# Kernel tuning notes

Hardware: AMD Instinct MI355X
Metric: run time of the kernel (lower is better)

The kernel has to match this reference:

```python
import jax, jax.numpy as jnp
import numpy as np

B, Hd, Wd, C, NH, WS = 8, 128, 128, 192, 6, 8
HDIM = int(C * 2.0)   # FFN hidden = 384
RED = C // 8          # AIM channel-gate reduction = 24


def setup_inputs() -> dict:
    key = jax.random.key(0)
    ks = jax.random.split(key, 12)
    s = 0.02
    return {
        "x": jax.random.normal(ks[0], (B, Hd * Wd, C), jnp.float32),
        "H": Hd,
        "W": Wd,
        "n1_w": jnp.ones((C,), jnp.float32),
        "n1_b": jnp.zeros((C,), jnp.float32),
        "qkv_w": jax.random.normal(ks[1], (C, 3 * C), jnp.float32) * s,
        "proj_w": jax.random.normal(ks[2], (C, C), jnp.float32) * s,
        "proj_b": jnp.zeros((C,), jnp.float32),
        "attn_bias": jax.random.normal(ks[3], (NH, WS * WS, WS * WS), jnp.float32) * s,
        "conv_w": jax.random.normal(ks[4], (C, 1, 3, 3), jnp.float32) * s,
        "cg_w1": jax.random.normal(ks[5], (RED, C), jnp.float32) * s,
        "cg_w2": jax.random.normal(ks[6], (C, RED), jnp.float32) * s,
        "n2_w": jnp.ones((C,), jnp.float32),
        "n2_b": jnp.zeros((C,), jnp.float32),
        "fc1_w": jax.random.normal(ks[7], (C, HDIM), jnp.float32) * s,
        "smix_w": jax.random.normal(ks[8], (HDIM, 1, 3, 3), jnp.float32) * s,
        "fc2_w": jax.random.normal(ks[9], (HDIM, C), jnp.float32) * s,
    }


def _ln(x, w, b):
    m = x.mean(-1, keepdims=True)
    v = ((x - m) ** 2).mean(-1, keepdims=True)
    return (x - m) * jax.lax.rsqrt(v + 1e-5) * w + b


def _dwconv(x, w, H, W):
    # x: [B, L, Cx] -> depthwise 3x3 'same' conv -> [B, L, Cx]
    Bx, L, Cx = x.shape
    xi = x.transpose(0, 2, 1).reshape(Bx, Cx, H, W)
    y = jax.lax.conv_general_dilated(
        xi, w, (1, 1), 'SAME', feature_group_count=Cx,
        dimension_numbers=('NCHW', 'OIHW', 'NCHW'))
    return y.reshape(Bx, Cx, L).transpose(0, 2, 1)


def _window_attn(x, H, W, qkv_w, proj_w, proj_b, bias):
    Bx, L, Cx = x.shape
    nHw, nWw = H // WS, W // WS  # H, W are multiples of WS here (no padding needed)
    hd = Cx // NH
    # [B, L, C] -> [B*nH*nW, ws*ws, C]
    xw = (x.reshape(Bx, nHw, WS, nWw, WS, Cx)
           .transpose(0, 1, 3, 2, 4, 5)
           .reshape(Bx * nHw * nWw, WS * WS, Cx))
    qkv = (xw @ qkv_w).reshape(-1, WS * WS, 3, NH, hd).transpose(2, 0, 3, 1, 4)
    q, k, v = qkv[0], qkv[1], qkv[2]          # [Bw, nh, N, hd]
    logits = (q * hd ** -0.5) @ k.transpose(0, 1, 3, 2) + bias[None]
    attn = jax.nn.softmax(logits, axis=-1)
    out = (attn @ v).transpose(0, 2, 1, 3).reshape(-1, WS * WS, Cx)
    out = out @ proj_w + proj_b
    # windows -> [B, L, C]
    return (out.reshape(Bx, nHw, nWw, WS, WS, Cx)
               .transpose(0, 1, 3, 2, 4, 5)
               .reshape(Bx, L, Cx))


def reference(x, H, W, n1_w, n1_b, qkv_w, proj_w, proj_b, attn_bias,
              conv_w, cg_w1, cg_w2, n2_w, n2_b, fc1_w, smix_w, fc2_w):
    n1 = _ln(x, n1_w, n1_b)
    attn_feat = _window_attn(n1, H, W, qkv_w, proj_w, proj_b, attn_bias)
    conv_feat = jax.nn.gelu(_dwconv(n1, conv_w, H, W), approximate=False)
    # AIM: channel_modulates_spatial (btype == 'spatial')
    pooled = conv_feat.mean(axis=1)                                   # [B, C]
    cm = jax.nn.sigmoid(jax.nn.gelu(pooled @ cg_w1.T, approximate=False) @ cg_w2.T)
    x = x + attn_feat * cm[:, None, :] + conv_feat                    # residual (DropPath=id)
    # FFN with depthwise spatial mixing
    n2 = _ln(x, n2_w, n2_b)
    h = jax.nn.gelu(n2 @ fc1_w, approximate=False)                    # [B, L, HDIM]
    h = _dwconv(h, smix_w, H, W)
    return x + h @ fc2_w
```

## Files before the change

### kernel.cpp

```cpp
#include <hip/hip_runtime.h>
#include <hip/hip_bf16.h>
#include <math.h>

#define BATCH 8
#define CCH 192
#define LTOK 16384
#define BL 131072LL
#define NWIN 2048
#define NHEADS 6

typedef __hip_bfloat16 bf16;
typedef __bf16 bfr;
typedef bfr bf16x8 __attribute__((ext_vector_type(8)));
typedef float f32x4 __attribute__((ext_vector_type(4)));
typedef unsigned short u16x8 __attribute__((ext_vector_type(8)));
typedef unsigned short u16x4 __attribute__((ext_vector_type(4)));
typedef unsigned int u32x2 __attribute__((ext_vector_type(2)));

#define FX     0
#define FN1W   1
#define FN1B   2
#define FQKVW  3
#define FPROJW 4
#define FPROJB 5
#define FBIAS  6
#define FCONVW 7
#define FCG1   8
#define FCG2   9
#define FN2W   10
#define FN2B   11
#define FFC1   12
#define FSMIX  13
#define FFC2   14

struct InPtrs { const void* p[15]; int n[15]; };

__device__ __forceinline__ float ldin(const void* p, long long i, int f32) {
    return f32 ? ((const float*)p)[i]
               : __bfloat162float(((const bf16*)p)[i]);
}

__device__ __forceinline__ float bfcvt(unsigned short u) {
    return __uint_as_float((unsigned)u << 16);
}

__device__ __forceinline__ f32x4 ld4f(const void* p, long long i, int f32) {
    if (f32) return *(const f32x4*)((const float*)p + i);
    u16x4 v = *(const u16x4*)((const bf16*)p + i);
    f32x4 r;
    r[0] = bfcvt(v[0]); r[1] = bfcvt(v[1]); r[2] = bfcvt(v[2]); r[3] = bfcvt(v[3]);
    return r;
}
__device__ __forceinline__ f32x4 ld4b(const bf16* p, long long i) {
    u16x4 v = *(const u16x4*)(p + i);
    f32x4 r;
    r[0] = bfcvt(v[0]); r[1] = bfcvt(v[1]); r[2] = bfcvt(v[2]); r[3] = bfcvt(v[3]);
    return r;
}
__device__ __forceinline__ void st4b(bf16* p, long long i, f32x4 v) {
    union { bf16 h; unsigned short u; } cv;
    u16x4 o;
    cv.h = __float2bfloat16(v[0]); o[0] = cv.u;
    cv.h = __float2bfloat16(v[1]); o[1] = cv.u;
    cv.h = __float2bfloat16(v[2]); o[2] = cv.u;
    cv.h = __float2bfloat16(v[3]); o[3] = cv.u;
    *(u16x4*)(p + i) = o;
}

__device__ __forceinline__ unsigned pk2bf(float a, float b) {
    union { bf16 h; unsigned short u; } ca, cb;
    ca.h = __float2bfloat16(a);
    cb.h = __float2bfloat16(b);
    return (unsigned)ca.u | ((unsigned)cb.u << 16);
}

__device__ __forceinline__ float gelu_f(float v) {
    return 0.5f * v * (1.0f + erff(v * 0.70710678118654752f));
}

__global__ void probe_k(InPtrs in, int* flags) {
    __shared__ int s_insane, s_evennz, s_oddnz;
    if (threadIdx.x == 0) { s_insane = 0; s_evennz = 0; s_oddnz = 0; }
    __syncthreads();
    int t = blockIdx.x;
    const bf16* p = (const bf16*)in.p[t];
    int n = in.n[t];
    int m = n < 2048 ? n : 2048;
    bool insane = false, evennz = false, oddnz = false;
    for (int i = threadIdx.x; i < m; i += 256) {
        float v = __bfloat162float(p[i]);
        if (!(fabsf(v) <= 1e9f)) insane = true;
        if (v != 0.0f) { if (i & 1) oddnz = true; else evennz = true; }
    }
    if (insane) s_insane = 1;
    if (evennz) s_evennz = 1;
    if (oddnz)  s_oddnz = 1;
    __syncthreads();
    if (threadIdx.x == 0)
        flags[t] = (s_insane || (!s_evennz && s_oddnz)) ? 1 : 0;
}

__global__ void transpose_k(const void* __restrict__ W, bf16* __restrict__ WT,
                            int K, int N, const int* flag) {
    int f = *flag;
    int idx = blockIdx.x * 256 + threadIdx.x;
    if (idx >= K * N) return;
    int k = idx / N, n = idx % N;
    WT[(long long)n * K + k] = __float2bfloat16(ldin(W, idx, f));
}

__global__ void convw_k(const void* __restrict__ W, float* __restrict__ WT,
                        int CX, const int* flag) {
    int f = *flag;
    int idx = blockIdx.x * 256 + threadIdx.x;
    if (idx >= CX * 9) return;
    int c = idx / 9, t = idx - c * 9;
    WT[t * CX + c] = ldin(W, idx, f);
}

__global__ __launch_bounds__(256)
void ln_kernel(const void* __restrict__ x, const void* __restrict__ w,
               const void* __restrict__ b, bf16* __restrict__ out,
               const int* flags) {
    int fx = flags[FX], fw = flags[FN1W], fb = flags[FN1B];
    int wv = threadIdx.x >> 6, lane = threadIdx.x & 63;
    int gw = lane >> 4, l16 = lane & 15;
    long long t = (long long)blockIdx.x * 16 + wv * 4 + gw;
    long long base = t * CCH;
    f32x4 v[3];
#pragma unroll
    for (int k = 0; k < 3; ++k)
        v[k] = ld4f(x, base + l16 * 4 + 64 * k, fx);
    float s = 0.f;
#pragma unroll
    for (int k = 0; k < 3; ++k) s += v[k][0] + v[k][1] + v[k][2] + v[k][3];
    s += __shfl_xor(s, 1); s += __shfl_xor(s, 2);
    s += __shfl_xor(s, 4); s += __shfl_xor(s, 8);
    float mean = s * (1.0f / 192.0f);
    float vs = 0.f;
#pragma unroll
    for (int k = 0; k < 3; ++k)
#pragma unroll
        for (int j = 0; j < 4; ++j) {
            float d = v[k][j] - mean;
            vs += d * d;
        }
    vs += __shfl_xor(vs, 1); vs += __shfl_xor(vs, 2);
    vs += __shfl_xor(vs, 4); vs += __shfl_xor(vs, 8);
    float rstd = rsqrtf(vs * (1.0f / 192.0f) + 1e-5f);
#pragma unroll
    for (int k = 0; k < 3; ++k) {
        int c0 = l16 * 4 + 64 * k;
        f32x4 wv4 = ld4f(w, c0, fw);
        f32x4 bv4 = ld4f(b, c0, fb);
        f32x4 o;
#pragma unroll
        for (int j = 0; j < 4; ++j)
            o[j] = (v[k][j] - mean) * rstd * wv4[j] + bv4[j];
        st4b(out, base + c0, o);
    }
}

template<int EPI, int KK, int NN, typename CT>
__global__ __launch_bounds__(256)
void gemm2_k(const bf16* __restrict__ A_, const bf16* __restrict__ BT_,
             CT* __restrict__ Cmat, const void* __restrict__ bias,
             const float* __restrict__ res, const int* __restrict__ flags) {
    constexpr int KT = KK / 192;
    constexpr int NC = NN / 64;
    constexpr int NITER = NC * KT;
    constexpr int GSTR = KK * 2;
    __shared__ __align__(16) char Ts[64 * 384];

    const int fb = (EPI == 1) ? flags[FPROJB] : 0;
    const int tid = threadIdx.x;
    const int lane = tid & 63, wv = tid >> 6;
    const int r16 = lane & 15, q = lane >> 4;
    const long long m0 = (long long)blockIdx.x * 64;
    const int swz = (r16 & 7) << 4;

    f32x4 pre[6];
    auto loadB = [&](int itn) {
        int nc2 = itn / KT, kt2 = itn - nc2 * KT;
#pragma unroll
        for (int p = 0; p < 6; ++p) {
            int off = p * 4096 + tid * 16;
            int row = off / 384, col = off - row * 384;
            pre[p] = *(const f32x4*)((const char*)BT_ +
                     (long long)(nc2 * 64 + row) * GSTR + kt2 * 384 + col);
        }
    };
    auto writeT = [&]() {
#pragma unroll
        for (int p = 0; p < 6; ++p) {
            int off = p * 4096 + tid * 16;
            int row = off / 384, col = off - row * 384;
            *(f32x4*)(Ts + row * 384 + (col ^ ((row & 7) << 4))) = pre[p];
        }
    };

    loadB(0);

    bf16x8 afrag[KK / 32];
    const char* Arow = Ts + (wv * 16 + r16) * 384;
    const char* asrc = (const char*)(A_ + m0 * KK);
#pragma unroll
    for (int kt = 0; kt < KT; ++kt) {
#pragma unroll
        for (int p = 0; p < 6; ++p) {
            int off = p * 4096 + tid * 16;
            int row = off / 384, col = off - row * 384;
            *(f32x4*)(Ts + row * 384 + (col ^ ((row & 7) << 4))) =
                *(const f32x4*)(asrc + (long long)row * GSTR + kt * 384 + col);
        }
        __syncthreads();
#pragma unroll
        for (int ks = 0; ks < 6; ++ks)
            afrag[kt * 6 + ks] = *(const bf16x8*)(Arow + ((ks * 64 + q * 16) ^ swz));
        __syncthreads();
    }
    writeT();
    __syncthreads();

    f32x4 acc0, acc1, acc2, acc3;
    float resv[16];

    for (int it = 0; it < NITER; ++it) {
        const int nc = it / KT, kt = it - nc * KT;
        if (kt == 0) {
            acc0 = f32x4{0.f, 0.f, 0.f, 0.f};
            acc1 = acc0; acc2 = acc0; acc3 = acc0;
            if (EPI == 3) {
#pragma unroll
                for (int j = 0; j < 4; ++j)
#pragma unroll
                    for (int r = 0; r < 4; ++r)
                        resv[j * 4 + r] =
                            res[(m0 + wv * 16 + q * 4 + r) * NN + nc * 64 + j * 16 + r16];
            }
        }
        const bool nxt = (it + 1 < NITER);
        if (nxt) loadB(it + 1);
#pragma unroll
        for (int ks = 0; ks < 6; ++ks) {
            bf16x8 a = afrag[kt * 6 + ks];
            const char* bb = Ts + r16 * 384 + ((ks * 64 + q * 16) ^ swz);
            bf16x8 b0 = *(const bf16x8*)(bb);
            bf16x8 b1 = *(const bf16x8*)(bb + 16 * 384);
            bf16x8 b2 = *(const bf16x8*)(bb + 32 * 384);
            bf16x8 b3 = *(const bf16x8*)(bb + 48 * 384);
            acc0 = __builtin_amdgcn_mfma_f32_16x16x32_bf16(a, b0, acc0, 0, 0, 0);
            acc1 = __builtin_amdgcn_mfma_f32_16x16x32_bf16(a, b1, acc1, 0, 0, 0);
            acc2 = __builtin_amdgcn_mfma_f32_16x16x32_bf16(a, b2, acc2, 0, 0, 0);
            acc3 = __builtin_amdgcn_mfma_f32_16x16x32_bf16(a, b3, acc3, 0, 0, 0);
        }
        __syncthreads();
        if (nxt) writeT();
        if (kt == KT - 1) {
            f32x4 accs[4] = {acc0, acc1, acc2, acc3};
#pragma unroll
            for (int j = 0; j < 4; ++j) {
                int col = nc * 64 + j * 16 + r16;
#pragma unroll
                for (int r = 0; r < 4; ++r) {
                    long long row = m0 + wv * 16 + q * 4 + r;
                    float v = accs[j][r];
                    if (EPI == 1) v += ldin(bias, col, fb);
                    if (EPI == 2) v = gelu_f(v);
                    if (EPI == 3) v += resv[j * 4 + r];
                    Cmat[row * NN + col] = (CT)v;
                }
            }
        }
        if (nxt) __syncthreads();
    }
}

__global__ __launch_bounds__(384)
void attn_proj_k(const bf16* __restrict__ qkv, const void* __restrict__ bias,
                 const bf16* __restrict__ pwT, const void* __restrict__ proj_b,
                 bf16* __restrict__ attnf, const int* __restrict__ flags) {
    __shared__ __align__(16) bfr Vt[6][32][64];
    __shared__ __align__(16) char PbRaw[6 * 64 * 144];

    const int fbias = flags[FBIAS];
    const int h = threadIdx.x >> 6, lane = threadIdx.x & 63;
    const int w = blockIdx.x;
    const int b = w >> 8, rem = w & 255, wy = rem >> 4, wx = rem & 15;
    const int l15 = lane & 15, quad = lane >> 4;
    const long long tokbase = (long long)b * LTOK + (wy * 8) * 128 + wx * 8;

    bfr (*Pb)[72] = (bfr(*)[72])(PbRaw + h * 64 * 144);

    long long vt = tokbase + (lane >> 3) * 128 + (lane & 7);
    const bfr* vp = (const bfr*)(qkv + vt * 576 + 384 + h * 32);
    bf16x8 v0 = *(const bf16x8*)(vp);
    bf16x8 v1 = *(const bf16x8*)(vp + 8);
    bf16x8 v2 = *(const bf16x8*)(vp + 16);
    bf16x8 v3 = *(const bf16x8*)(vp + 24);

    bf16x8 aq[4], bk[4];
#pragma unroll
    for (int mt = 0; mt < 4; ++mt) {
        int i0 = mt * 16 + l15;
        long long t = tokbase + (i0 >> 3) * 128 + (i0 & 7);
        const bfr* qp = (const bfr*)(qkv + t * 576 + h * 32 + quad * 8);
        aq[mt] = *(const bf16x8*)qp;
        bk[mt] = *(const bf16x8*)(qp + 192);
    }

#pragma unroll
    for (int j = 0; j < 8; ++j) {
        int sc = lane ^ (j << 3);
        Vt[h][j][sc]      = v0[j];
        Vt[h][j + 8][sc]  = v1[j];
        Vt[h][j + 16][sc] = v2[j];
        Vt[h][j + 24][sc] = v3[j];
    }

    f32x4 T[4][4];
#pragma unroll
    for (int ti = 0; ti < 4; ++ti)
#pragma unroll
        for (int tj = 0; tj < 4; ++tj) {
            f32x4 z = {0.f, 0.f, 0.f, 0.f};
            T[ti][tj] = __builtin_amdgcn_mfma_f32_16x16x32_bf16(bk[ti], aq[tj], z, 0, 0, 0);
        }

    const float scale = 0.17677669529663689f;
    const long long bias0 = (long long)h * 4096;
#pragma unroll
    for (int tj = 0; tj < 4; ++tj) {
        const long long brow = bias0 + (tj * 16 + l15) * 64 + quad * 4;
        float mloc = -3.0e38f;
#pragma unroll
        for (int ti = 0; ti < 4; ++ti) {
            f32x4 bv4 = ld4f(bias, brow + ti * 16, fbias);
#pragma unroll
            for (int r = 0; r < 4; ++r) {
                float v = T[ti][tj][r] * scale + bv4[r];
                T[ti][tj][r] = v;
                mloc = fmaxf(mloc, v);
            }
        }
        mloc = fmaxf(mloc, __shfl_xor(mloc, 16));
        mloc = fmaxf(mloc, __shfl_xor(mloc, 32));
        float l = 0.f;
#pragma unroll
        for (int ti = 0; ti < 4; ++ti)
#pragma unroll
            for (int r = 0; r < 4; ++r) {
                float e = __expf(T[ti][tj][r] - mloc);
                T[ti][tj][r] = e;
                l += e;
            }
        l += __shfl_xor(l, 16);
        l += __shfl_xor(l, 32);
        float linv = 1.0f / l;
#pragma unroll
        for (int ti = 0; ti < 4; ++ti) {
            unsigned wlo = pk2bf(T[ti][tj][0] * linv, T[ti][tj][1] * linv);
            unsigned whi = pk2bf(T[ti][tj][2] * linv, T[ti][tj][3] * linv);
            *(u32x2*)&Pb[tj * 16 + l15][ti * 16 + quad * 4] = u32x2{wlo, whi};
        }
    }

    __syncthreads();

    f32x4 O[4][2];
#pragma unroll
    for (int tj = 0; tj < 4; ++tj)
#pragma unroll
        for (int n2 = 0; n2 < 2; ++n2)
            O[tj][n2] = f32x4{0.f, 0.f, 0.f, 0.f};
    const int vsw = (l15 & 7) << 3;
#pragma unroll
    for (int kc = 0; kc < 2; ++kc) {
        bf16x8 bv0 = *(const bf16x8*)&Vt[h][l15][(kc * 32 + quad * 8) ^ vsw];
        bf16x8 bv1 = *(const bf16x8*)&Vt[h][16 + l15][(kc * 32 + quad * 8) ^ vsw];
#pragma unroll
        for (int tj = 0; tj < 4; ++tj) {
            bf16x8 ap = *(const bf16x8*)&Pb[tj * 16 + l15][kc * 32 + quad * 8];
            O[tj][0] = __builtin_amdgcn_mfma_f32_16x16x32_bf16(ap, bv0, O[tj][0], 0, 0, 0);
            O[tj][1] = __builtin_amdgcn_mfma_f32_16x16x32_bf16(ap, bv1, O[tj][1], 0, 0, 0);
        }
    }

    __syncthreads();

    bf16* cat = (bf16*)PbRaw;
#pragma unroll
    for (int tj = 0; tj < 4; ++tj)
#pragma unroll
        for (int n2 = 0; n2 < 2; ++n2)
#pragma unroll
            for (int r = 0; r < 4; ++r)
                cat[(tj * 16 + quad * 4 + r) * 200 + h * 32 + n2 * 16 + l15] =
                    __float2bfloat16(O[tj][n2][r]);

    __syncthreads();

    const int fpb = flags[FPROJB];
    f32x4 pacc[4][2];
#pragma unroll
    for (int mt = 0; mt < 4; ++mt) {
        pacc[mt][0] = f32x4{0.f, 0.f, 0.f, 0.f};
        pacc[mt][1] = pacc[mt][0];
    }
#pragma unroll
    for (int ks = 0; ks < 6; ++ks) {
        bf16x8 af[4];
#pragma unroll
        for (int mt = 0; mt < 4; ++mt)
            af[mt] = *(const bf16x8*)&cat[(mt * 16 + l15) * 200 + ks * 32 + quad * 8];
#pragma unroll
        for (int nt = 0; nt < 2; ++nt) {
            int col = h * 32 + nt * 16 + l15;
            bf16x8 bfr8 = *(const bf16x8*)((const bfr*)pwT + (long long)col * 192 + ks * 32 + quad * 8);
#pragma unroll
            for (int mt = 0; mt < 4; ++mt)
                pacc[mt][nt] = __builtin_amdgcn_mfma_f32_16x16x32_bf16(af[mt], bfr8, pacc[mt][nt], 0, 0, 0);
        }
    }

#pragma unroll
    for (int nt = 0; nt < 2; ++nt) {
        int col = h * 32 + nt * 16 + l15;
        float bv = ldin(proj_b, col, fpb);
#pragma unroll
        for (int mt = 0; mt < 4; ++mt)
#pragma unroll
            for (int r = 0; r < 4; ++r) {
                long long row = (long long)w * 64 + mt * 16 + quad * 4 + r;
                attnf[row * CCH + col] = __float2bfloat16(pacc[mt][nt][r] + bv);
            }
    }
}

template<bool GELU, int CX>
__global__ __launch_bounds__(256)
void dwconv_s4_k(const bf16* __restrict__ in, const float* __restrict__ wt,
                 bf16* __restrict__ out) {
    constexpr int CG = CX / 8;
    int cpx = gridDim.x >> 3;
    int lb = (blockIdx.x & 7) * cpx + (blockIdx.x >> 3);
    long long idx = (long long)lb * 256 + threadIdx.x;
    if (idx >= (BL / 4) * CG) return;
    int cg = (int)(idx % CG);
    long long s = idx / CG;
    int xs = (int)(s & 31);
    long long by = s >> 5;
    int y = (int)(by & 127);
    int x0 = xs * 4;
    int c0 = cg * 8;
    const long long rowpix = by * 128;

    float acc[4][8] = {};
#pragma unroll
    for (int dy = -1; dy <= 1; ++dy) {
        int yy = y + dy;
        if (yy < 0 || yy > 127) continue;
        const bf16* rp = in + ((rowpix + dy * 128) + x0) * CX + c0;
        float fcol[6][8];
#pragma unroll
        for (int ci = 0; ci < 6; ++ci) {
            int xx = x0 + ci - 1;
            if (xx < 0 || xx > 127) {
#pragma unroll
                for (int j = 0; j < 8; ++j) fcol[ci][j] = 0.f;
            } else {
                u16x8 v = *(const u16x8*)(rp + (ci - 1) * CX);
#pragma unroll
                for (int j = 0; j < 8; ++j) fcol[ci][j] = bfcvt(v[j]);
            }
        }
        const float* wb = wt + (dy + 1) * 3 * CX + c0;
#pragma unroll
        for (int dx = 0; dx < 3; ++dx) {
            f32x4 w0 = *(const f32x4*)(wb + dx * CX);
            f32x4 w1 = *(const f32x4*)(wb + dx * CX + 4);
#pragma unroll
            for (int px = 0; px < 4; ++px) {
#pragma unroll
                for (int j = 0; j < 4; ++j) {
                    acc[px][j]     += fcol[px + dx][j]     * w0[j];
                    acc[px][j + 4] += fcol[px + dx][j + 4] * w1[j];
                }
            }
        }
    }
#pragma unroll
    for (int px = 0; px < 4; ++px) {
        __attribute__((aligned(16))) unsigned short ob[8];
#pragma unroll
        for (int j = 0; j < 8; ++j) {
            float vv = acc[px][j];
            if (GELU) vv = gelu_f(vv);
            union { bf16 h; unsigned short u; } cv;
            cv.h = __float2bfloat16(vv);
            ob[j] = cv.u;
        }
        *(u16x8*)(out + (rowpix + x0 + px) * CX + c0) = *(const u16x8*)ob;
    }
}

__global__ __launch_bounds__(192)
void pool_k(const bf16* __restrict__ conv, float* __restrict__ pooled) {
    __shared__ float red[8][192];
    int b = blockIdx.x, chunk = blockIdx.y;
    int cg = threadIdx.x % 24, rr = threadIdx.x / 24;
    float acc[8] = {0.f, 0.f, 0.f, 0.f, 0.f, 0.f, 0.f, 0.f};
    long long rowbase = (long long)b * LTOK + chunk * 256;
    for (int r = rr; r < 256; r += 8) {
        u16x8 v = *(const u16x8*)(conv + (rowbase + r) * CCH + cg * 8);
#pragma unroll
        for (int j = 0; j < 8; ++j) acc[j] += bfcvt(v[j]);
    }
#pragma unroll
    for (int j = 0; j < 8; ++j) red[rr][cg * 8 + j] = acc[j];
    __syncthreads();
    if (rr == 0) {
#pragma unroll
        for (int j = 0; j < 8; ++j) {
            float s = 0.f;
#pragma unroll
            for (int i = 0; i < 8; ++i) s += red[i][cg * 8 + j];
            atomicAdd(&pooled[b * CCH + cg * 8 + j], s);
        }
    }
}

__global__ void cm_k(const float* __restrict__ pooled, const void* __restrict__ w1,
                     const void* __restrict__ w2, float* __restrict__ cm,
                     const int* flags) {
    __shared__ float ps[192], g[24];
    int f1 = flags[FCG1], f2 = flags[FCG2];
    int b = blockIdx.x, c = threadIdx.x;
    ps[c] = pooled[b * CCH + c] * (1.0f / 16384.0f);
    __syncthreads();
    if (c < 24) {
        float t = 0.f;
        for (int k = 0; k < 192; ++k) t += ps[k] * ldin(w1, c * 192 + k, f1);
        g[c] = gelu_f(t);
    }
    __syncthreads();
    float s = 0.f;
#pragma unroll
    for (int r = 0; r < 24; ++r) s += g[r] * ldin(w2, c * 24 + r, f2);
    cm[b * CCH + c] = 1.0f / (1.0f + expf(-s));
}

__global__ __launch_bounds__(256)
void x2ln2_k(const void* __restrict__ x, const bf16* __restrict__ attnf,
             const bf16* __restrict__ conv, const float* __restrict__ cm,
             const void* __restrict__ w, const void* __restrict__ bb,
             float* __restrict__ x2, bf16* __restrict__ n2, const int* flags) {
    int fx = flags[FX], fw = flags[FN2W], fb = flags[FN2B];
    int wv = threadIdx.x >> 6, lane = threadIdx.x & 63;
    int gw = lane >> 4, l16 = lane & 15;
    long long t = (long long)blockIdx.x * 16 + wv * 4 + gw;
    int b = (int)(t >> 14);
    int l = (int)(t & 16383);
    int y = l >> 7, xx = l & 127;
    long long wrow = ((long long)b * 256 + (y >> 3) * 16 + (xx >> 3)) * 64 + (y & 7) * 8 + (xx & 7);

    f32x4 sv[3];
#pragma unroll
    for (int k = 0; k < 3; ++k) {
        int c0 = l16 * 4 + 64 * k;
        f32x4 xv  = ld4f(x, t * CCH + c0, fx);
        f32x4 af  = ld4b(attnf, wrow * CCH + c0);
        f32x4 cf  = ld4b(conv, t * CCH + c0);
        f32x4 cmv = *(const f32x4*)(cm + b * CCH + c0);
        f32x4 o;
#pragma unroll
        for (int j = 0; j < 4; ++j)
            o[j] = xv[j] + af[j] * cmv[j] + cf[j];
        *(f32x4*)(x2 + t * CCH + c0) = o;
        sv[k] = o;
    }
    float s = 0.f;
#pragma unroll
    for (int k = 0; k < 3; ++k) s += sv[k][0] + sv[k][1] + sv[k][2] + sv[k][3];
    s += __shfl_xor(s, 1); s += __shfl_xor(s, 2);
    s += __shfl_xor(s, 4); s += __shfl_xor(s, 8);
    float mean = s * (1.0f / 192.0f);
    float vs = 0.f;
#pragma unroll
    for (int k = 0; k < 3; ++k)
#pragma unroll
        for (int j = 0; j < 4; ++j) {
            float d = sv[k][j] - mean;
            vs += d * d;
        }
    vs += __shfl_xor(vs, 1); vs += __shfl_xor(vs, 2);
    vs += __shfl_xor(vs, 4); vs += __shfl_xor(vs, 8);
    float rstd = rsqrtf(vs * (1.0f / 192.0f) + 1e-5f);
#pragma unroll
    for (int k = 0; k < 3; ++k) {
        int c0 = l16 * 4 + 64 * k;
        f32x4 wv4 = ld4f(w, c0, fw);
        f32x4 bv4 = ld4f(bb, c0, fb);
        f32x4 o;
#pragma unroll
        for (int j = 0; j < 4; ++j)
            o[j] = (sv[k][j] - mean) * rstd * wv4[j] + bv4[j];
        st4b(n2, t * CCH + c0, o);
    }
}

extern "C" void kernel_launch(void* const* d_in, const int* in_sizes, int n_in,
                              void* d_out, int out_size, void* d_ws, size_t ws_size,
                              hipStream_t stream) {
    (void)n_in; (void)out_size; (void)ws_size;
    float* out = (float*)d_out;

    char* wsp = (char*)d_ws;
    size_t off = 0;
    auto alloc = [&](size_t bytes) -> char* {
        char* p = wsp + off;
        off += (bytes + 255) & ~(size_t)255;
        return p;
    };
    int*  flags   = (int*)alloc(15 * 4);
    bf16* qkv_wT  = (bf16*)alloc(576 * 192 * 2);
    bf16* proj_wT = (bf16*)alloc(192 * 192 * 2);
    bf16* fc1_wT  = (bf16*)alloc(384 * 192 * 2);
    bf16* fc2_wT  = (bf16*)alloc(192 * 384 * 2);
    float* convwT = (float*)alloc(9 * CCH * 4);
    float* smixwT = (float*)alloc(9 * 384 * 4);
    float* pooled = (float*)alloc(BATCH * CCH * 4);
    float* cm     = (float*)alloc(BATCH * CCH * 4);
    char* Rbig    = alloc(BL * 576 * 2);
    char* Rpair   = alloc(BL * 384 * 2);

    bf16* qkvb  = (bf16*)Rbig;
    bf16* convf = (bf16*)Rbig;
    bf16* hbuf  = (bf16*)Rbig;
    bf16* n1    = (bf16*)Rpair;
    bf16* attnf = (bf16*)(Rpair + (size_t)BL * 192 * 2);
    bf16* n2    = n1;
    bf16* h2    = (bf16*)Rpair;
    float* x2   = out;

    const int imap[15] = {0, 3, 4, 5, 6, 7, 8, 9, 10, 11, 12, 13, 14, 15, 16};
    InPtrs ip;
    for (int i = 0; i < 15; ++i) { ip.p[i] = d_in[imap[i]]; ip.n[i] = in_sizes[imap[i]]; }
    const void* x        = d_in[0];
    const void* qkv_w    = d_in[5];
    const void* proj_w   = d_in[6];
    const void* proj_b   = d_in[7];
    const void* attnbias = d_in[8];
    const void* conv_w   = d_in[9];
    const void* cg_w1    = d_in[10];
    const void* cg_w2    = d_in[11];
    const void* fc1_w    = d_in[14];
    const void* smix_w   = d_in[15];
    const void* fc2_w    = d_in[16];

    probe_k<<<15, 256, 0, stream>>>(ip, flags);

    transpose_k<<<(192 * 576 + 255) / 256, 256, 0, stream>>>(qkv_w, qkv_wT, 192, 576, flags + FQKVW);
    transpose_k<<<(192 * 192 + 255) / 256, 256, 0, stream>>>(proj_w, proj_wT, 192, 192, flags + FPROJW);
    transpose_k<<<(192 * 384 + 255) / 256, 256, 0, stream>>>(fc1_w, fc1_wT, 192, 384, flags + FFC1);
    transpose_k<<<(384 * 192 + 255) / 256, 256, 0, stream>>>(fc2_w, fc2_wT, 384, 192, flags + FFC2);
    convw_k<<<(CCH * 9 + 255) / 256, 256, 0, stream>>>(conv_w, convwT, CCH, flags + FCONVW);
    convw_k<<<(384 * 9 + 255) / 256, 256, 0, stream>>>(smix_w, smixwT, 384, flags + FSMIX);
    hipMemsetAsync(pooled, 0, BATCH * CCH * 4, stream);

    ln_kernel<<<BL / 16, 256, 0, stream>>>(x, d_in[3], d_in[4], n1, flags);
    gemm2_k<0, 192, 576, bf16><<<BL / 64, 256, 0, stream>>>(n1, qkv_wT, qkvb, nullptr, nullptr, flags);
    attn_proj_k<<<NWIN, 384, 0, stream>>>(qkvb, attnbias, proj_wT, proj_b, attnf, flags);
    dwconv_s4_k<true, 192><<<(int)(BL / 4 * 24 / 256), 256, 0, stream>>>(n1, convwT, convf);
    pool_k<<<dim3(BATCH, 64), 192, 0, stream>>>(convf, pooled);
    cm_k<<<BATCH, 192, 0, stream>>>(pooled, cg_w1, cg_w2, cm, flags);
    x2ln2_k<<<BL / 16, 256, 0, stream>>>(x, attnf, convf, cm, d_in[12], d_in[13], x2, n2, flags);
    gemm2_k<2, 192, 384, bf16><<<BL / 64, 256, 0, stream>>>(n2, fc1_wT, hbuf, nullptr, nullptr, flags);
    dwconv_s4_k<false, 384><<<(int)(BL / 4 * 48 / 256), 256, 0, stream>>>(hbuf, smixwT, h2);
    gemm2_k<3, 384, 192, float><<<BL / 64, 256, 0, stream>>>(h2, fc2_wT, out, nullptr, x2, flags);
}
```

Before: 618.6 us.

## Keep softmax probabilities in registers via shuffles and shrink attention LDS footprint

The attention kernel no longer writes the softmax probability matrix to shared memory. It repacks the bf16 probabilities into the MFMA A-operand layout with cross-lane shuffles, which removes one block-wide barrier and the P round-trip through LDS. The V tile and the concatenated head output now share a single 24KB buffer, and the concat buffer uses an XOR swizzle in place of padding. The smaller LDS footprint may allow more blocks per CU, at the cost of extra shuffle instructions and register pressure from the held probability values.

```diff
diff --git a/kernel.cpp b/kernel.cpp
--- a/kernel.cpp
+++ b/kernel.cpp
@@ -280,8 +280,7 @@
 void attn_proj_k(const bf16* __restrict__ qkv, const void* __restrict__ bias,
                  const bf16* __restrict__ pwT, const void* __restrict__ proj_b,
                  bf16* __restrict__ attnf, const int* __restrict__ flags) {
-    __shared__ __align__(16) bfr Vt[6][32][64];
-    __shared__ __align__(16) char PbRaw[6 * 64 * 144];
+    __shared__ __align__(16) char SM[24576];
 
     const int fbias = flags[FBIAS];
     const int h = threadIdx.x >> 6, lane = threadIdx.x & 63;
@@ -289,8 +288,7 @@
     const int b = w >> 8, rem = w & 255, wy = rem >> 4, wx = rem & 15;
     const int l15 = lane & 15, quad = lane >> 4;
     const long long tokbase = (long long)b * LTOK + (wy * 8) * 128 + wx * 8;
-
-    bfr (*Pb)[72] = (bfr(*)[72])(PbRaw + h * 64 * 144);
+    bfr* vtp = (bfr*)(SM + h * 4096);
 
     long long vt = tokbase + (lane >> 3) * 128 + (lane & 7);
     const bfr* vp = (const bfr*)(qkv + vt * 576 + 384 + h * 32);
@@ -312,10 +310,10 @@
 #pragma unroll
     for (int j = 0; j < 8; ++j) {
         int sc = lane ^ (j << 3);
-        Vt[h][j][sc]      = v0[j];
-        Vt[h][j + 8][sc]  = v1[j];
-        Vt[h][j + 16][sc] = v2[j];
-        Vt[h][j + 24][sc] = v3[j];
+        vtp[j * 64 + sc]        = v0[j];
+        vtp[(j + 8) * 64 + sc]  = v1[j];
+        vtp[(j + 16) * 64 + sc] = v2[j];
+        vtp[(j + 24) * 64 + sc] = v3[j];
     }
 
     f32x4 T[4][4];
@@ -329,6 +327,7 @@
 
     const float scale = 0.17677669529663689f;
     const long long bias0 = (long long)h * 4096;
+    unsigned Wreg[4][4][2];
 #pragma unroll
     for (int tj = 0; tj < 4; ++tj) {
         const long long brow = bias0 + (tj * 16 + l15) * 64 + quad * 4;
@@ -359,48 +358,58 @@
         float linv = 1.0f / l;
 #pragma unroll
         for (int ti = 0; ti < 4; ++ti) {
-            unsigned wlo = pk2bf(T[ti][tj][0] * linv, T[ti][tj][1] * linv);
-            unsigned whi = pk2bf(T[ti][tj][2] * linv, T[ti][tj][3] * linv);
-            *(u32x2*)&Pb[tj * 16 + l15][ti * 16 + quad * 4] = u32x2{wlo, whi};
-        }
-    }
-
-    __syncthreads();
-
+            Wreg[tj][ti][0] = pk2bf(T[ti][tj][0] * linv, T[ti][tj][1] * linv);
+            Wreg[tj][ti][1] = pk2bf(T[ti][tj][2] * linv, T[ti][tj][3] * linv);
+        }
+    }
+
+    const int vsw = (l15 & 7) << 3;
+    bf16x8 bv[2][2];
+#pragma unroll
+    for (int kc = 0; kc < 2; ++kc) {
+        bv[kc][0] = *(const bf16x8*)&vtp[l15 * 64 + ((kc * 32 + quad * 8) ^ vsw)];
+        bv[kc][1] = *(const bf16x8*)&vtp[(16 + l15) * 64 + ((kc * 32 + quad * 8) ^ vsw)];
+    }
+    const int hi = quad >> 1, qlow = quad & 1;
     f32x4 O[4][2];
 #pragma unroll
+    for (int tj = 0; tj < 4; ++tj) {
+        O[tj][0] = f32x4{0.f, 0.f, 0.f, 0.f};
+        O[tj][1] = O[tj][0];
+    }
+#pragma unroll
     for (int tj = 0; tj < 4; ++tj)
 #pragma unroll
+        for (int kc = 0; kc < 2; ++kc) {
+            union { unsigned u[4]; bf16x8 v; } ap;
+#pragma unroll
+            for (int j2 = 0; j2 < 4; ++j2) {
+                int srcl = (2 * qlow + (j2 >> 1)) * 16 + l15;
+                unsigned va = (unsigned)__shfl((int)Wreg[tj][2 * kc][j2 & 1], srcl);
+                unsigned vb = (unsigned)__shfl((int)Wreg[tj][2 * kc + 1][j2 & 1], srcl);
+                ap.u[j2] = hi ? vb : va;
+            }
+            O[tj][0] = __builtin_amdgcn_mfma_f32_16x16x32_bf16(ap.v, bv[kc][0], O[tj][0], 0, 0, 0);
+            O[tj][1] = __builtin_amdgcn_mfma_f32_16x16x32_bf16(ap.v, bv[kc][1], O[tj][1], 0, 0, 0);
+        }
+
+    __syncthreads();
+
+#pragma unroll
+    for (int tj = 0; tj < 4; ++tj)
+#pragma unroll
         for (int n2 = 0; n2 < 2; ++n2)
-            O[tj][n2] = f32x4{0.f, 0.f, 0.f, 0.f};
-    const int vsw = (l15 & 7) << 3;
-#pragma unroll
-    for (int kc = 0; kc < 2; ++kc) {
-        bf16x8 bv0 = *(const bf16x8*)&Vt[h][l15][(kc * 32 + quad * 8) ^ vsw];
-        bf16x8 bv1 = *(const bf16x8*)&Vt[h][16 + l15][(kc * 32 + quad * 8) ^ vsw];
-#pragma unroll
-        for (int tj = 0; tj < 4; ++tj) {
-            bf16x8 ap = *(const bf16x8*)&Pb[tj * 16 + l15][kc * 32 + quad * 8];
-            O[tj][0] = __builtin_amdgcn_mfma_f32_16x16x32_bf16(ap, bv0, O[tj][0], 0, 0, 0);
-            O[tj][1] = __builtin_amdgcn_mfma_f32_16x16x32_bf16(ap, bv1, O[tj][1], 0, 0, 0);
-        }
-    }
-
-    __syncthreads();
-
-    bf16* cat = (bf16*)PbRaw;
-#pragma unroll
-    for (int tj = 0; tj < 4; ++tj)
-#pragma unroll
-        for (int n2 = 0; n2 < 2; ++n2)
-#pragma unroll
-            for (int r = 0; r < 4; ++r)
-                cat[(tj * 16 + quad * 4 + r) * 200 + h * 32 + n2 * 16 + l15] =
-                    __float2bfloat16(O[tj][n2][r]);
+#pragma unroll
+            for (int r = 0; r < 4; ++r) {
+                int row = tj * 16 + quad * 4 + r;
+                int cb = (h * 64 + n2 * 32 + l15 * 2) ^ ((row & 7) << 4);
+                *(bf16*)(SM + row * 384 + cb) = __float2bfloat16(O[tj][n2][r]);
+            }
 
     __syncthreads();
 
     const int fpb = flags[FPROJB];
+    const int csw = (l15 & 7) << 4;
     f32x4 pacc[4][2];
 #pragma unroll
     for (int mt = 0; mt < 4; ++mt) {
@@ -412,27 +421,28 @@
         bf16x8 af[4];
 #pragma unroll
         for (int mt = 0; mt < 4; ++mt)
-            af[mt] = *(const bf16x8*)&cat[(mt * 16 + l15) * 200 + ks * 32 + quad * 8];
+            af[mt] = *(const bf16x8*)(SM + (mt * 16 + l15) * 384 +
+                                      ((ks * 64 + quad * 16) ^ csw));
 #pragma unroll
         for (int nt = 0; nt < 2; ++nt) {
             int col = h * 32 + nt * 16 + l15;
-            bf16x8 bfr8 = *(const bf16x8*)((const bfr*)pwT + (long long)col * 192 + ks * 32 + quad * 8);
+            bf16x8 bw = *(const bf16x8*)((const bfr*)pwT + (long long)col * 192 + ks * 32 + quad * 8);
 #pragma unroll
             for (int mt = 0; mt < 4; ++mt)
-                pacc[mt][nt] = __builtin_amdgcn_mfma_f32_16x16x32_bf16(af[mt], bfr8, pacc[mt][nt], 0, 0, 0);
+                pacc[mt][nt] = __builtin_amdgcn_mfma_f32_16x16x32_bf16(af[mt], bw, pacc[mt][nt], 0, 0, 0);
         }
     }
 
 #pragma unroll
     for (int nt = 0; nt < 2; ++nt) {
         int col = h * 32 + nt * 16 + l15;
-        float bv = ldin(proj_b, col, fpb);
+        float bv2 = ldin(proj_b, col, fpb);
 #pragma unroll
         for (int mt = 0; mt < 4; ++mt)
 #pragma unroll
             for (int r = 0; r < 4; ++r) {
                 long long row = (long long)w * 64 + mt * 16 + quad * 4 + r;
-                attnf[row * CCH + col] = __float2bfloat16(pacc[mt][nt][r] + bv);
+                attnf[row * CCH + col] = __float2bfloat16(pacc[mt][nt][r] + bv2);
             }
     }
 }
```

Result: no change. 612.6 us (-1.0%).
